# Performance work log

Hardware: AMD Instinct MI355X
Metric: run time of the kernel (lower is better)

Reference implementation:

```python
import jax, jax.numpy as jnp
import numpy as np

B, L, D = 4, 4096, 1024


def setup_inputs() -> dict:
    key = jax.random.key(0)
    ks = jax.random.split(key, 10)
    s = 1.0 / np.sqrt(D)  # torch Linear default init scale
    return {
        "x": jax.random.normal(ks[0], (B, L, D), dtype=jnp.float32),
        "hidden": jax.random.normal(ks[1], (B, D), dtype=jnp.float32),
        "W_ln_z": jax.random.uniform(ks[2], (D, D), jnp.float32, -s, s),
        "b_ln_z": jax.random.uniform(ks[3], (D,), jnp.float32, -s, s),
        "W_dt": jax.random.uniform(ks[4], (D, D), jnp.float32, -s, s),
        "b_dt": jax.random.uniform(ks[5], (D,), jnp.float32, -s, s),
        "W_y": jax.random.uniform(ks[6], (D, D), jnp.float32, -s, s),
        "b_y": jax.random.uniform(ks[7], (D,), jnp.float32, -s, s),
        "W_g": jax.random.uniform(ks[8], (D, D), jnp.float32, -s, s),
        "b_g": jax.random.uniform(ks[9], (D,), jnp.float32, -s, s),
    }


def reference(x, hidden, W_ln_z, b_ln_z, W_dt, b_dt, W_y, b_y, W_g, b_g):
    # Linear projections (torch Linear: x @ W.T + b)
    z_pre = x @ W_ln_z.T + b_ln_z          # (B, L, D)
    dt_pre = x @ W_dt.T + b_dt             # (B, L, D)

    # -softplus(-u) == log_sigmoid(u)
    ln_z = jax.nn.log_sigmoid(z_pre)       # ln z
    ln_da = jax.nn.log_sigmoid(dt_pre)     # ln(delta*a)
    ln_z_da = ln_z + ln_da
    ln_o_da = jax.nn.log_sigmoid(-dt_pre)  # -softplus(dt_pre)

    ln_o_da_cumsum = jnp.cumsum(ln_o_da, axis=1)
    # log-space parallel scan: h_t = sum_{s<=t} z_s*da_s * prod_{s<r<=t} o_da_r
    lcse = jax.lax.cumlogsumexp(ln_z_da - ln_o_da_cumsum, axis=1)
    h_inner = jnp.exp(lcse + ln_o_da_cumsum)                       # (B, L, D)
    h_cross = jnp.exp(ln_o_da_cumsum) * hidden[:, None, :]         # (B, L, D)
    h = h_inner + h_cross

    gate = jax.nn.silu(x @ W_g.T + b_g)
    y = (h @ W_y.T + b_y) * gate
    return y, h
```

## Files before the change

### kernel.cpp

```cpp
#include <hip/hip_runtime.h>


#define BDIM 4
#define LDIM 4096
#define DDIM 1024
#define MROWS (BDIM * LDIM)
#define KDIM 1024
#define NPROJ 3072
#define NCHUNK 64
#define LCHUNK 64

typedef __attribute__((ext_vector_type(8))) short short8v;
typedef __attribute__((ext_vector_type(4))) float f32x4;
typedef unsigned int uint;

__device__ __forceinline__ float bf2f(short u) {
    union { float f; uint i; } v;
    v.i = ((uint)(unsigned short)u) << 16;
    return v.f;
}
__device__ __forceinline__ short f2bf(float f) {
    union { float f; uint i; } v; v.f = f;
    uint r = v.i + 0x7FFFu + ((v.i >> 16) & 1u);
    return (short)(r >> 16);
}
__device__ __forceinline__ float sigf(float x) { return 1.f / (1.f + __expf(-x)); }

#define SCANSTEP(zz, dd, H0, H1, A0, A1, DO_A)                                     \
  {                                                                                \
    float _z0 = bf2f((short)((zz) & 0xffff)), _z1 = bf2f((short)((zz) >> 16));     \
    float _d0 = bf2f((short)((dd) & 0xffff)), _d1 = bf2f((short)((dd) >> 16));     \
    float _e0 = __expf(-_d0), _r0 = 1.f / (1.f + _e0);                             \
    float _o0 = _e0 * _r0, _q0 = sigf(_z0) * _r0;                                  \
    float _e1 = __expf(-_d1), _r1 = 1.f / (1.f + _e1);                             \
    float _o1 = _e1 * _r1, _q1 = sigf(_z1) * _r1;                                  \
    H0 = _q0 + _o0 * H0; H1 = _q1 + _o1 * H1;                                      \
    if (DO_A) { A0 *= _o0; A1 *= _o1; }                                            \
  }

__global__ void cast_f32_bf16(const float* __restrict__ src, short* __restrict__ dst, int n4) {
    int i = blockIdx.x * blockDim.x + threadIdx.x;
    int stride = gridDim.x * blockDim.x;
    for (; i < n4; i += stride) {
        float4 v = reinterpret_cast<const float4*>(src)[i];
        short4 o;
        o.x = f2bf(v.x); o.y = f2bf(v.y); o.z = f2bf(v.z); o.w = f2bf(v.w);
        reinterpret_cast<short4*>(dst)[i] = o;
    }
}

__global__ void cast4_f32_bf16(const float* __restrict__ s0, const float* __restrict__ s1,
                               const float* __restrict__ s2, const float* __restrict__ s3,
                               short* __restrict__ dst) {
    int i = blockIdx.x * blockDim.x + threadIdx.x;
    int seg = i >> 18, off = i & ((1 << 18) - 1);
    const float* s = (seg == 0) ? s0 : (seg == 1) ? s1 : (seg == 2) ? s2 : s3;
    float4 v = reinterpret_cast<const float4*>(s)[off];
    short4 o;
    o.x = f2bf(v.x); o.y = f2bf(v.y); o.z = f2bf(v.z); o.w = f2bf(v.w);
    reinterpret_cast<short4*>(dst)[i] = o;
}

#define STAGE(arr, gbase, half, kofs)                                              \
  do {                                                                             \
    _Pragma("unroll")                                                              \
    for (int _i = 0; _i < 2; ++_i) {                                               \
      int _c = _i * 512 + tid;                                                     \
      int _row = _c >> 3, _g = _c & 7;                                             \
      int _gsw = _g ^ (_row & 7);                                                  \
      __builtin_amdgcn_global_load_lds(                                            \
        (const __attribute__((address_space(1))) void*)(                           \
            (gbase) + (size_t)((half) * 128 + _row) * K + (kofs) + _gsw * 8),      \
        (__attribute__((address_space(3))) void*)(                                 \
            &arr[(_i * 512 + wid * 64) * 8]),                                      \
        16, 0, 0);                                                                 \
    }                                                                              \
  } while (0)

#define LDA4(dst, arr)                                                             \
  _Pragma("unroll")                                                                \
  for (int _m = 0; _m < 4; ++_m) {                                                 \
    int _r = _m * 32 + wm * 16 + lrow;                                             \
    _Pragma("unroll")                                                              \
    for (int _kk = 0; _kk < 2; ++_kk)                                              \
      dst[_m][_kk] = *(const short8v*)&arr[_r * 64 +                               \
                       (((_kk * 4 + kq) ^ (lrow & 7)) * 8)];                       \
  }

#define LDB2(dst, arr)                                                             \
  _Pragma("unroll")                                                                \
  for (int _n = 0; _n < 2; ++_n) {                                                 \
    int _r = _n * 64 + wn * 16 + lrow;                                             \
    _Pragma("unroll")                                                              \
    for (int _kk = 0; _kk < 2; ++_kk)                                              \
      dst[_n][_kk] = *(const short8v*)&arr[_r * 64 +                               \
                       (((_kk * 4 + kq) ^ (lrow & 7)) * 8)];                       \
  }

#define MFMAQ(mi0, ni0, afr, bfr)                                                  \
  __builtin_amdgcn_s_setprio(1);                                                   \
  _Pragma("unroll")                                                                \
  for (int _kk = 0; _kk < 2; ++_kk)                                                \
    _Pragma("unroll")                                                              \
    for (int _m = 0; _m < 4; ++_m)                                                 \
      _Pragma("unroll")                                                            \
      for (int _n = 0; _n < 2; ++_n)                                               \
        acc[(mi0) + _m][(ni0) + _n] = __builtin_amdgcn_mfma_f32_16x16x32_bf16(     \
            afr[_m][_kk], bfr[_n][_kk], acc[(mi0) + _m][(ni0) + _n], 0, 0, 0);     \
  __builtin_amdgcn_s_setprio(0);

#define BARB()   __builtin_amdgcn_s_barrier()
#define VM4()    asm volatile("s_waitcnt vmcnt(4)")
#define VM0()    asm volatile("s_waitcnt vmcnt(0)")

template<int OUT_BF16, int HAS_GATE>
__global__ __launch_bounds__(512, 2) void gemm256(
    const short* __restrict__ A, const short* __restrict__ Bm,
    const float* __restrict__ bias, void* __restrict__ Cv,
    int M, int N, int K,
    const short* __restrict__ gate, int ldg)
{
    __shared__ short As0h0[8192], As0h1[8192], As1h0[8192], As1h1[8192];
    __shared__ short Bs0h0[8192], Bs0h1[8192], Bs1h0[8192], Bs1h1[8192];

    const int tid  = threadIdx.x;
    const int lane = tid & 63;
    const int wid  = tid >> 6;
    const int wm   = wid >> 2;
    const int wn   = wid & 3;
    const int lrow = lane & 15;
    const int kq   = lane >> 4;

    const int gx  = gridDim.x;
    const int nwg = gx * gridDim.y;
    int flat = blockIdx.y * gx + blockIdx.x;
    if ((nwg & 7) == 0) { int q = nwg >> 3; flat = (flat & 7) * q + (flat >> 3); }
    const int m0 = (flat / gx) * 256;
    const int n0 = (flat % gx) * 256;

    const short* Abase = A + (size_t)m0 * K;
    const short* Bbase = Bm + (size_t)n0 * K;

    f32x4 acc[8][4];
#pragma unroll
    for (int i = 0; i < 8; ++i)
#pragma unroll
        for (int j = 0; j < 4; ++j)
            acc[i][j] = (f32x4){0.f, 0.f, 0.f, 0.f};

    STAGE(As0h0, Abase, 0, 0);
    STAGE(As0h1, Abase, 1, 0);
    STAGE(Bs0h0, Bbase, 0, 0);
    STAGE(Bs0h1, Bbase, 1, 0);
    STAGE(As1h0, Abase, 0, 64);
    STAGE(Bs1h0, Bbase, 0, 64);
    VM4(); BARB();

    const int NT = K / 64;
    for (int t = 0; t < NT; t += 2) {
        const int k1 = (t + 1) * 64, k2 = (t + 2) * 64, k3 = (t + 3) * 64;
        const bool more = (t + 2) < NT;
        short8v af[4][2], b0[2][2], b1[2][2];

        LDA4(af, As0h0) LDB2(b0, Bs0h0)
        STAGE(As1h1, Abase, 1, k1);
        BARB(); MFMAQ(0, 0, af, b0)

        LDB2(b1, Bs0h1)
        STAGE(Bs1h1, Bbase, 1, k1);
        BARB(); MFMAQ(0, 2, af, b1)

        LDA4(af, As0h1)
        if (more) STAGE(As0h0, Abase, 0, k2);
        BARB(); MFMAQ(4, 2, af, b1)

        if (more) { STAGE(Bs0h0, Bbase, 0, k2); VM4(); } else { VM0(); }
        BARB(); MFMAQ(4, 0, af, b0)

        LDA4(af, As1h0) LDB2(b0, Bs1h0)
        if (more) STAGE(As0h1, Abase, 1, k2);
        BARB(); MFMAQ(0, 0, af, b0)

        LDB2(b1, Bs1h1)
        if (more) STAGE(Bs0h1, Bbase, 1, k2);
        BARB(); MFMAQ(0, 2, af, b1)

        LDA4(af, As1h1)
        if (more) STAGE(As1h0, Abase, 0, k3);
        BARB(); MFMAQ(4, 2, af, b1)

        if (more) { STAGE(Bs1h0, Bbase, 0, k3); VM4(); }
        BARB(); MFMAQ(4, 0, af, b0)
    }

    const int lr4 = (lane >> 4) * 4;
#pragma unroll
    for (int mi = 0; mi < 8; ++mi) {
        int rowb = m0 + mi * 32 + wm * 16 + lr4;
#pragma unroll
        for (int ni = 0; ni < 4; ++ni) {
            int col = n0 + ni * 64 + wn * 16 + lrow;
            float bv = bias[col];
#pragma unroll
            for (int r = 0; r < 4; ++r) {
                int row = rowb + r;
                float val = acc[mi][ni][r] + bv;
                if (HAS_GATE) {
                    float g = bf2f(gate[(size_t)row * ldg + col]);
                    val *= g * sigf(g);
                }
                if (OUT_BF16)
                    ((short*)Cv)[(size_t)row * N + col] = f2bf(val);
                else
                    ((float*)Cv)[(size_t)row * N + col] = val;
            }
        }
    }
}

__global__ __launch_bounds__(256) void chunk_reduce(
    const short* __restrict__ pre, float* __restrict__ sA, float* __restrict__ sBv)
{
    const int t = threadIdx.x;
    const int c = blockIdx.x;
    const int b = blockIdx.y;
    const int d0 = blockIdx.z * 512 + 2 * t;
    float A0 = 1.f, A1 = 1.f, B0 = 0.f, B1 = 0.f;
    size_t base = ((size_t)(b * LDIM) + c * LCHUNK) * NPROJ + d0;
    for (int i = 0; i < LCHUNK; i += 4) {
        uint z0 = *(const uint*)&pre[base];
        uint d_0 = *(const uint*)&pre[base + DDIM];
        uint z1 = *(const uint*)&pre[base + NPROJ];
        uint d_1 = *(const uint*)&pre[base + NPROJ + DDIM];
        uint z2 = *(const uint*)&pre[base + 2 * NPROJ];
        uint d_2 = *(const uint*)&pre[base + 2 * NPROJ + DDIM];
        uint z3 = *(const uint*)&pre[base + 3 * NPROJ];
        uint d_3 = *(const uint*)&pre[base + 3 * NPROJ + DDIM];
        SCANSTEP(z0, d_0, B0, B1, A0, A1, 1)
        SCANSTEP(z1, d_1, B0, B1, A0, A1, 1)
        SCANSTEP(z2, d_2, B0, B1, A0, A1, 1)
        SCANSTEP(z3, d_3, B0, B1, A0, A1, 1)
        base += 4 * NPROJ;
    }
    int idx = ((b * NCHUNK + c) << 10) + d0;
    *reinterpret_cast<float2*>(&sA[idx])  = make_float2(A0, A1);
    *reinterpret_cast<float2*>(&sBv[idx]) = make_float2(B0, B1);
}

__global__ __launch_bounds__(1024) void chunk_prefix(
    const float* __restrict__ sA, const float* __restrict__ sBv,
    const float* __restrict__ hidden, float* __restrict__ sI)
{
    const int d = threadIdx.x;
    const int b = blockIdx.x;
    float h = hidden[b * DDIM + d];
    int idx = (b * NCHUNK << 10) + d;
    for (int c = 0; c < NCHUNK; c += 4) {
        float a0 = sA[idx];            float v0 = sBv[idx];
        float a1 = sA[idx + 1024];     float v1 = sBv[idx + 1024];
        float a2 = sA[idx + 2048];     float v2 = sBv[idx + 2048];
        float a3 = sA[idx + 3072];     float v3 = sBv[idx + 3072];
        sI[idx]        = h; h = v0 + a0 * h;
        sI[idx + 1024] = h; h = v1 + a1 * h;
        sI[idx + 2048] = h; h = v2 + a2 * h;
        sI[idx + 3072] = h; h = v3 + a3 * h;
        idx += 4096;
    }
}

__global__ __launch_bounds__(256) void chunk_apply(
    const short* __restrict__ pre, const float* __restrict__ sI,
    float* __restrict__ hout, short* __restrict__ hbf)
{
    const int t = threadIdx.x;
    const int c = blockIdx.x;
    const int b = blockIdx.y;
    const int d0 = blockIdx.z * 512 + 2 * t;
    float2 hi = *reinterpret_cast<const float2*>(&sI[((b * NCHUNK + c) << 10) + d0]);
    float h0 = hi.x, h1 = hi.y;
    size_t base  = ((size_t)(b * LDIM) + c * LCHUNK) * NPROJ + d0;
    size_t obase = ((size_t)(b * LDIM) + c * LCHUNK) * DDIM + d0;
    for (int i = 0; i < LCHUNK; i += 4) {
        uint z0 = *(const uint*)&pre[base];
        uint d_0 = *(const uint*)&pre[base + DDIM];
        uint z1 = *(const uint*)&pre[base + NPROJ];
        uint d_1 = *(const uint*)&pre[base + NPROJ + DDIM];
        uint z2 = *(const uint*)&pre[base + 2 * NPROJ];
        uint d_2 = *(const uint*)&pre[base + 2 * NPROJ + DDIM];
        uint z3 = *(const uint*)&pre[base + 3 * NPROJ];
        uint d_3 = *(const uint*)&pre[base + 3 * NPROJ + DDIM];
        float dummyA = 0.f, dummyB = 0.f;
#define EMIT(HH0, HH1, off)                                                        \
        *reinterpret_cast<float2*>(&hout[obase + (off) * DDIM]) =                  \
            make_float2(HH0, HH1);                                                 \
        *reinterpret_cast<uint*>(&hbf[obase + (off) * DDIM]) =                     \
            ((uint)(unsigned short)f2bf(HH0)) |                                    \
            (((uint)(unsigned short)f2bf(HH1)) << 16);
        SCANSTEP(z0, d_0, h0, h1, dummyA, dummyB, 0) EMIT(h0, h1, 0)
        SCANSTEP(z1, d_1, h0, h1, dummyA, dummyB, 0) EMIT(h0, h1, 1)
        SCANSTEP(z2, d_2, h0, h1, dummyA, dummyB, 0) EMIT(h0, h1, 2)
        SCANSTEP(z3, d_3, h0, h1, dummyA, dummyB, 0) EMIT(h0, h1, 3)
#undef EMIT
        base += 4 * NPROJ;
        obase += 4 * DDIM;
    }
}

extern "C" void kernel_launch(void* const* d_in, const int* in_sizes, int n_in,
                              void* d_out, int out_size, void* d_ws, size_t ws_size,
                              hipStream_t stream) {
    const float* x      = (const float*)d_in[0];
    const float* hidden = (const float*)d_in[1];
    const float* W_ln_z = (const float*)d_in[2];
    const float* b_ln_z = (const float*)d_in[3];
    const float* W_dt   = (const float*)d_in[4];
    const float* b_dt   = (const float*)d_in[5];
    const float* W_y    = (const float*)d_in[6];
    const float* b_y    = (const float*)d_in[7];
    const float* W_g    = (const float*)d_in[8];
    const float* b_g    = (const float*)d_in[9];

    char* ws = (char*)d_ws;
    short* x_bf   = (short*)(ws + 0);
    short* Wcat   = (short*)(ws + 33554432);
    short* Wy_bf  = (short*)(ws + 39845888);
    float* biascat= (float*)(ws + 41943040);
    short* pre    = (short*)(ws + 41955328);
    float* sA     = (float*)(ws + 142618624);
    float* sBv    = (float*)(ws + 143667200);
    float* sI     = (float*)(ws + 144715776);

    cast_f32_bf16<<<2048, 256, 0, stream>>>(x, x_bf, (MROWS * KDIM) / 4);
    cast4_f32_bf16<<<4096, 256, 0, stream>>>(W_ln_z, W_dt, W_g, W_y, Wcat);

    hipMemcpyAsync(biascat,            b_ln_z, DDIM * sizeof(float), hipMemcpyDeviceToDevice, stream);
    hipMemcpyAsync(biascat + DDIM,     b_dt,   DDIM * sizeof(float), hipMemcpyDeviceToDevice, stream);
    hipMemcpyAsync(biascat + 2 * DDIM, b_g,    DDIM * sizeof(float), hipMemcpyDeviceToDevice, stream);

    gemm256<1, 0><<<dim3(NPROJ / 256, MROWS / 256), 512, 0, stream>>>(
        x_bf, Wcat, biascat, pre, MROWS, NPROJ, KDIM, nullptr, 0);

    float* y_out = (float*)d_out;
    float* h_out = (float*)d_out + (size_t)MROWS * DDIM;
    short* h_bf  = x_bf;
    chunk_reduce<<<dim3(NCHUNK, BDIM, 2), 256, 0, stream>>>(pre, sA, sBv);
    chunk_prefix<<<dim3(BDIM), 1024, 0, stream>>>(sA, sBv, hidden, sI);
    chunk_apply<<<dim3(NCHUNK, BDIM, 2), 256, 0, stream>>>(pre, sI, h_out, h_bf);

    gemm256<0, 1><<<dim3(DDIM / 256, MROWS / 256), 512, 0, stream>>>(
        h_bf, Wy_bf, b_y, y_out, MROWS, DDIM, KDIM, pre + 2 * DDIM, NPROJ);
}
```

Before: 253.2 us.

## Software-pipeline LDS fragment loads ahead of MFMAs with double-buffered registers

```diff
diff --git a/kernel.cpp b/kernel.cpp
--- a/kernel.cpp
+++ b/kernel.cpp
@@ -60,6 +60,7 @@
     o.x = f2bf(v.x); o.y = f2bf(v.y); o.z = f2bf(v.z); o.w = f2bf(v.w);
     reinterpret_cast<short4*>(dst)[i] = o;
 }
+
 
 #define STAGE(arr, gbase, half, kofs)                                              \
   do {                                                                             \
@@ -112,6 +113,7 @@
 #define BARB()   __builtin_amdgcn_s_barrier()
 #define VM4()    asm volatile("s_waitcnt vmcnt(4)")
 #define VM0()    asm volatile("s_waitcnt vmcnt(0)")
+#define SCHEDB() __builtin_amdgcn_sched_barrier(0)
 
 template<int OUT_BF16, int HAS_GATE>
 __global__ __launch_bounds__(512, 2) void gemm256(
@@ -148,6 +150,8 @@
         for (int j = 0; j < 4; ++j)
             acc[i][j] = (f32x4){0.f, 0.f, 0.f, 0.f};
 
+    short8v afA[4][2], afB[4][2], bA1[2][2], bA2[2][2], bB[2][2];
+
     STAGE(As0h0, Abase, 0, 0);
     STAGE(As0h1, Abase, 1, 0);
     STAGE(Bs0h0, Bbase, 0, 0);
@@ -155,42 +159,46 @@
     STAGE(As1h0, Abase, 0, 64);
     STAGE(Bs1h0, Bbase, 0, 64);
     VM4(); BARB();
+    LDA4(afA, As0h0) LDB2(bA1, Bs0h0)
+    SCHEDB();
 
     const int NT = K / 64;
     for (int t = 0; t < NT; t += 2) {
         const int k1 = (t + 1) * 64, k2 = (t + 2) * 64, k3 = (t + 3) * 64;
         const bool more = (t + 2) < NT;
-        short8v af[4][2], b0[2][2], b1[2][2];
-
-        LDA4(af, As0h0) LDB2(b0, Bs0h0)
+
+        LDB2(bB, Bs0h1) SCHEDB();
+        MFMAQ(0, 0, afA, bA1)
         STAGE(As1h1, Abase, 1, k1);
-        BARB(); MFMAQ(0, 0, af, b0)
-
-        LDB2(b1, Bs0h1)
+        LDA4(afB, As0h1) SCHEDB();
+        BARB();
+        MFMAQ(0, 2, afA, bB)
         STAGE(Bs1h1, Bbase, 1, k1);
-        BARB(); MFMAQ(0, 2, af, b1)
-
-        LDA4(af, As0h1)
+        VM4(); BARB();
+        LDA4(afA, As1h0) SCHEDB();
+        MFMAQ(4, 2, afB, bB)
         if (more) STAGE(As0h0, Abase, 0, k2);
-        BARB(); MFMAQ(4, 2, af, b1)
-
-        if (more) { STAGE(Bs0h0, Bbase, 0, k2); VM4(); } else { VM0(); }
-        BARB(); MFMAQ(4, 0, af, b0)
-
-        LDA4(af, As1h0) LDB2(b0, Bs1h0)
+        LDB2(bA2, Bs1h0) SCHEDB();
+        BARB();
+        MFMAQ(4, 0, afB, bA1)
+        if (more) STAGE(Bs0h0, Bbase, 0, k2);
+        VM4(); BARB();
+        LDB2(bB, Bs1h1) SCHEDB();
+        MFMAQ(0, 0, afA, bA2)
         if (more) STAGE(As0h1, Abase, 1, k2);
-        BARB(); MFMAQ(0, 0, af, b0)
-
-        LDB2(b1, Bs1h1)
+        LDA4(afB, As1h1) SCHEDB();
+        BARB();
+        MFMAQ(0, 2, afA, bB)
         if (more) STAGE(Bs0h1, Bbase, 1, k2);
-        BARB(); MFMAQ(0, 2, af, b1)
-
-        LDA4(af, As1h1)
+        VM4(); BARB();
+        LDA4(afA, As0h0) SCHEDB();
+        MFMAQ(4, 2, afB, bB)
         if (more) STAGE(As1h0, Abase, 0, k3);
-        BARB(); MFMAQ(4, 2, af, b1)
-
-        if (more) { STAGE(Bs1h0, Bbase, 0, k3); VM4(); }
-        BARB(); MFMAQ(4, 0, af, b0)
+        LDB2(bA1, Bs0h0) SCHEDB();
+        BARB();
+        MFMAQ(4, 0, afB, bA2)
+        if (more) STAGE(Bs1h0, Bbase, 0, k3);
+        VM4(); BARB();
     }
 
     const int lr4 = (lane >> 4) * 4;
```

New measurement: 329.7 us. +30.2%, slower.
